# Performance work log

Hardware: AMD Instinct MI355X
Metric: run time of the kernel (lower is better)

The kernel has to match this reference:

```python
import jax, jax.numpy as jnp
import numpy as np

D_MODEL = 1024
N_HEADS = 16
HEAD_DIM = D_MODEL // N_HEADS  # 64


def _rotate_half(x):
    x1, x2 = jnp.split(x, 2, axis=-1)
    return jnp.concatenate((-x2, x1), axis=-1)


def setup_inputs() -> dict:
    key = jax.random.key(0)
    ks = jax.random.split(key, 9)
    B, S = 2, 2048
    sc = 1.0 / np.sqrt(D_MODEL)
    return {
        "x": jax.random.normal(ks[0], (B, S, D_MODEL), dtype=jnp.float32),
        "Wq": jax.random.normal(ks[1], (D_MODEL, D_MODEL), dtype=jnp.float32) * sc,
        "bq": jax.random.normal(ks[2], (D_MODEL,), dtype=jnp.float32) * 0.02,
        "Wk": jax.random.normal(ks[3], (D_MODEL, D_MODEL), dtype=jnp.float32) * sc,
        "bk": jax.random.normal(ks[4], (D_MODEL,), dtype=jnp.float32) * 0.02,
        "Wv": jax.random.normal(ks[5], (D_MODEL, D_MODEL), dtype=jnp.float32) * sc,
        "bv": jax.random.normal(ks[6], (D_MODEL,), dtype=jnp.float32) * 0.02,
        "Wo": jax.random.normal(ks[7], (D_MODEL, D_MODEL), dtype=jnp.float32) * sc,
        "bo": jax.random.normal(ks[8], (D_MODEL,), dtype=jnp.float32) * 0.02,
    }


def reference(x, Wq, bq, Wk, bk, Wv, bv, Wo, bo):
    B, S, _ = x.shape
    H, D = N_HEADS, HEAD_DIM
    # QKV projections -> [B, H, S, D]
    q = (x @ Wq + bq).reshape(B, S, H, D).transpose(0, 2, 1, 3)
    k = (x @ Wk + bk).reshape(B, S, H, D).transpose(0, 2, 1, 3)
    v = (x @ Wv + bv).reshape(B, S, H, D).transpose(0, 2, 1, 3)
    # Rotary embedding on head_dim
    inv_freq = 1.0 / (10000.0 ** (jnp.arange(0, D, 2, dtype=jnp.float32) / D))
    t = jnp.arange(S, dtype=jnp.float32)
    freqs = jnp.outer(t, inv_freq)                      # [S, D/2]
    emb = jnp.concatenate((freqs, freqs), axis=-1)      # [S, D]
    # Faithful to torch: cos/sin end up rank-5 [1,1,1,S,D], promoting q/k to [1,B,H,S,D]
    cos = jnp.cos(emb)[None, None, None]
    sin = jnp.sin(emb)[None, None, None]
    qe = q * cos + _rotate_half(q) * sin                # [1,B,H,S,D]
    ke = k * cos + _rotate_half(k) * sin                # [1,B,H,S,D]
    scores = jnp.matmul(qe, jnp.swapaxes(ke, -1, -2)) / np.sqrt(D).astype(np.float32)  # [1,B,H,S,S]
    attn = jax.nn.softmax(scores, axis=-1)
    out = jnp.matmul(attn, v)                           # [1,B,H,S,D] (v broadcast)
    # Faithful replication of torch transpose(1,2).contiguous().view(B,S,d_model)
    out = out.transpose(0, 2, 1, 3, 4).reshape(B, S, H * D)
    return out @ Wo + bo
```

## Files before the change

kernel.cpp:

```cpp
#include <hip/hip_runtime.h>
#include <hip/hip_bf16.h>
#include <stdint.h>

typedef __bf16 bf16;
typedef __bf16 bf16x8 __attribute__((ext_vector_type(8)));
typedef __bf16 bf16x4 __attribute__((ext_vector_type(4)));
typedef float  f32x4  __attribute__((ext_vector_type(4)));
typedef int    i32x4  __attribute__((ext_vector_type(4)));

#define MFMA16(a, b, c) __builtin_amdgcn_mfma_f32_16x16x32_bf16((a), (b), (c), 0, 0, 0)

#define GLOAD16(gp, lp) __builtin_amdgcn_global_load_lds(                     \
    (__attribute__((address_space(1))) void*)(gp),                            \
    (__attribute__((address_space(3))) void*)(lp), 16, 0, 0)


__global__ __launch_bounds__(256) void k_prep(
    const float* __restrict__ x,
    const float* __restrict__ Wq, const float* __restrict__ Wk,
    const float* __restrict__ Wv, const float* __restrict__ Wo,
    bf16* __restrict__ xb, bf16* __restrict__ wqkvt, bf16* __restrict__ wot,
    float* __restrict__ ct, float* __restrict__ st) {
    __shared__ float t[32][33];
    const int bid = blockIdx.x, tid = threadIdx.x;
    if (bid < 4096) {
        const int i = bid * 256 + tid;
        float4 v = ((const float4*)x)[i];
        bf16x4 o;
        o[0] = (bf16)v.x; o[1] = (bf16)v.y; o[2] = (bf16)v.z; o[3] = (bf16)v.w;
        ((bf16x4*)xb)[i] = o;
    } else if (bid < 4352) {
        const int i = (bid - 4096) * 256 + tid;
        const int s = i >> 5, j = i & 31;
        const float inv = expf(-(float)j * (9.210340371976184f / 32.0f));
        const float a = (float)s * inv;
        ct[i] = cosf(a);
        st[i] = sinf(a);
    } else {
        const int wb = bid - 4352;
        const int z = wb >> 10, tb = wb & 1023;
        const float* src = (z == 0) ? Wq : (z == 1) ? Wk : (z == 2) ? Wv : Wo;
        bf16* dst = (z < 3) ? wqkvt + (size_t)z * 1024 * 1024 : wot;
        const int bx = (tb & 31) * 32, by = (tb >> 5) * 32;
        const int tx = tid & 31, ty = tid >> 5;
#pragma unroll
        for (int i = 0; i < 32; i += 8)
            t[ty + i][tx] = src[(size_t)(by + ty + i) * 1024 + bx + tx];
        __syncthreads();
#pragma unroll
        for (int i = 0; i < 32; i += 8)
            dst[(size_t)(bx + ty + i) * 1024 + by + tx] = (bf16)t[tx][ty + i];
    }
}

__device__ __forceinline__ void gemm_loop(const bf16* __restrict__ A,
                                          const bf16* __restrict__ Bt,
                                          int m0, int n0,
                                          bf16* As, bf16* Bs,
                                          f32x4 (&acc)[4][4]) {
    const int tid  = threadIdx.x;
    const int w    = tid >> 6, lane = tid & 63;
    const int wr   = (w >> 1) * 64, wc = (w & 1) * 64;
    const int l15  = lane & 15, l4 = lane >> 4;
    const int srow = w * 16 + (lane >> 2);
    const int skol = 8 * ((lane & 3) ^ ((lane >> 3) & 3));
    const int rdb  = l15 * 32 + 8 * (l4 ^ ((l15 >> 1) & 3));
    const bf16* Ap = A  + (size_t)(m0 + srow) * 1024 + skol;
    const bf16* Bp = Bt + (size_t)(n0 + srow) * 1024 + skol;

#define GSTAGE(B, kt) do {                                                   \
        GLOAD16(Ap + (kt),         As + (B) * 4096 + w * 512);               \
        GLOAD16(Ap + 65536 + (kt), As + (B) * 4096 + 2048 + w * 512);        \
        GLOAD16(Bp + (kt),         Bs + (B) * 4096 + w * 512);               \
        GLOAD16(Bp + 65536 + (kt), Bs + (B) * 4096 + 2048 + w * 512);        \
    } while (0)

#define GTILE(t, B) do {                                                     \
        asm volatile("s_waitcnt vmcnt(0)" ::: "memory");                     \
        __builtin_amdgcn_s_barrier();                                        \
        if ((t) < 31) GSTAGE((B) ^ 1, ((t) + 1) * 32);                       \
        bf16x8 af[4], bfv[4];                                                \
        _Pragma("unroll")                                                    \
        for (int m = 0; m < 4; ++m)                                          \
            af[m] = *(const bf16x8*)(As + (B) * 4096 + (wr + 16 * m) * 32 + rdb); \
        _Pragma("unroll")                                                    \
        for (int n = 0; n < 4; ++n)                                          \
            bfv[n] = *(const bf16x8*)(Bs + (B) * 4096 + (wc + 16 * n) * 32 + rdb); \
        __builtin_amdgcn_s_setprio(1);                                       \
        _Pragma("unroll")                                                    \
        for (int m = 0; m < 4; ++m)                                          \
            _Pragma("unroll")                                                \
            for (int n = 0; n < 4; ++n)                                      \
                acc[m][n] = MFMA16(af[m], bfv[n], acc[m][n]);                \
        __builtin_amdgcn_s_setprio(0);                                       \
    } while (0)

    GSTAGE(0, 0);
    for (int t = 0; t < 32; t += 2) {
        GTILE(t, 0);
        GTILE(t + 1, 1);
    }
#undef GTILE
#undef GSTAGE
}

__global__ __launch_bounds__(256) void k_gemm_qkv(
    const bf16* __restrict__ X, const bf16* __restrict__ Wt,
    const float* __restrict__ bq, const float* __restrict__ bk,
    const float* __restrict__ bv,
    const float* __restrict__ ct, const float* __restrict__ st,
    bf16* __restrict__ qbuf, bf16* __restrict__ kbuf, bf16* __restrict__ vtb) {
    __shared__ __align__(16) bf16 As[2 * 4096];
    __shared__ __align__(16) bf16 Bs[2 * 4096];
    f32x4 acc[4][4] = {};
    const int nwg = gridDim.x * gridDim.y;
    const int wg  = blockIdx.y * gridDim.x + blockIdx.x;
    const int sw  = (wg & 7) * (nwg >> 3) + (wg >> 3);
    const int m0 = (sw / gridDim.x) * 128, n0 = (sw % gridDim.x) * 128;
    gemm_loop(X, Wt, m0, n0, As, Bs, acc);

    const int tid = threadIdx.x;
    const int w = tid >> 6, lane = tid & 63;
    const int wr = (w >> 1) * 64, wc = (w & 1) * 64;
    const int l15 = lane & 15, l4 = lane >> 4;

    const int featbase = n0 + wc;
    const int kind = featbase >> 10;
    const int col0 = featbase & 1023;
    const int h = col0 >> 6;
    const float* bias = (kind == 0) ? bq : (kind == 1) ? bk : bv;
    const float oscale = (kind == 0) ? 0.18033688011112042f : 1.0f;

#pragma unroll
    for (int m = 0; m < 4; ++m) {
#pragma unroll
        for (int j = 0; j < 4; ++j) {
            const int tok = m0 + wr + 16 * m + 4 * l4 + j;
            const int b = tok >> 11, s = tok & 2047;
            float vals[4];
#pragma unroll
            for (int n = 0; n < 4; ++n)
                vals[n] = acc[m][n][j] + bias[col0 + 16 * n + l15];
            if (kind < 2) {
                bf16* dst = (kind == 0) ? qbuf : kbuf;
                const size_t base = ((size_t)((b * 16 + h) * 2048 + s)) * 64;
#pragma unroll
                for (int n = 0; n < 4; ++n) {
                    const int dd = 16 * n + l15;
                    const int jr = dd & 31;
                    const float c = ct[s * 32 + jr], sn = st[s * 32 + jr];
                    const float other = vals[n ^ 2];
                    const float rot = (dd < 32) ? -other : other;
                    dst[base + dd] = (bf16)((vals[n] * c + rot * sn) * oscale);
                }
            } else {
                const int sp = (s & ~63) | ((s & 0x1C) << 1) | ((s & 0x20) >> 3) | (s & 3);
#pragma unroll
                for (int n = 0; n < 4; ++n) {
                    const int dd = 16 * n + l15;
                    vtb[((size_t)((b * 16 + h) * 64 + dd)) * 2048 + sp] = (bf16)vals[n];
                }
            }
        }
    }
}

__global__ __launch_bounds__(512) void k_attn(const bf16* __restrict__ qbuf,
                                              const bf16* __restrict__ kbuf,
                                              const bf16* __restrict__ vtb,
                                              bf16* __restrict__ ob) {
    __shared__ __align__(16) bf16 smem[2 * 2 * 2 * 4096];

    const int tid = threadIdx.x, w = tid >> 6, lane = tid & 63;
    const int team = w >> 2, wt = w & 3;
    const int l15 = lane & 15, l4 = lane >> 4;

    const int sid = blockIdx.x;
    const int bh  = (sid & 7) * 4 + ((sid >> 3) >> 4);
    const int qb0 = ((sid >> 3) & 15) * 128;
    const int b = bh >> 4, h = bh & 15;

    const bf16* qp = qbuf + ((size_t)bh * 2048 + qb0 + wt * 32 + l15) * 64 + 8 * l4;
    i32x4 qr00 = *(const i32x4*)qp;
    i32x4 qr01 = *(const i32x4*)(qp + 32);
    i32x4 qr10 = *(const i32x4*)(qp + 16 * 64);
    i32x4 qr11 = *(const i32x4*)(qp + 16 * 64 + 32);
    asm volatile("" :: "v"(qr00), "v"(qr01), "v"(qr10), "v"(qr11));
    asm volatile("s_waitcnt vmcnt(0)" ::: "memory");
    bf16x8 aq[2][2];
    aq[0][0] = __builtin_bit_cast(bf16x8, qr00);
    aq[0][1] = __builtin_bit_cast(bf16x8, qr01);
    aq[1][0] = __builtin_bit_cast(bf16x8, qr10);
    aq[1][1] = __builtin_bit_cast(bf16x8, qr11);

    bf16x8 ones;
#pragma unroll
    for (int i = 0; i < 8; ++i) ones[i] = (bf16)1.0f;

    f32x4 ao[2][4] = {};
    f32x4 lacc[2] = {};
    const f32x4 zf = {0.f, 0.f, 0.f, 0.f};

    const int r8   = lane >> 3;
    const int skol = 8 * ((lane & 7) ^ r8);
    const int rdb  = l15 * 64 + 32 * ((l15 >> 2) & 1) + 8 * (l4 ^ (l15 & 3));
    const bf16* kp = kbuf + (size_t)bh * 131072 + (size_t)team * 65536
                   + (size_t)(wt * 8 + r8) * 64 + skol;
    const bf16* vp = vtb  + (size_t)bh * 131072 + (size_t)(wt * 8 + r8) * 2048
                   + team * 1024 + skol;
    bf16* sK = smem + team * 16384;
    bf16* sV = smem + team * 16384 + 8192;
    const bf16* pK0 = sK + rdb;
    const bf16* pK1 = sK + (rdb ^ 32);
    const bf16* pV0 = sV + rdb;
    const bf16* pV1 = sV + (rdb ^ 32);

#define STAGE(B, t) do {                                                  \
        GLOAD16(kp + (size_t)(t) * 4096,        sK + (B) * 4096 + wt * 512);        \
        GLOAD16(kp + (size_t)(t) * 4096 + 2048, sK + (B) * 4096 + 2048 + wt * 512); \
        GLOAD16(vp + (t) * 64,                  sV + (B) * 4096 + wt * 512);        \
        GLOAD16(vp + 65536 + (t) * 64,          sV + (B) * 4096 + 2048 + wt * 512); \
    } while (0)

#define TILE(t, B) do {                                                       \
        asm volatile("s_waitcnt vmcnt(0)" ::: "memory");                      \
        __builtin_amdgcn_s_barrier();                                         \
        if ((t) < 15) STAGE((B) ^ 1, (t) + 1);                                \
        bf16x8 kfr[2][4], vfr[2][4];                                          \
        _Pragma("unroll")                                                     \
        for (int n = 0; n < 4; ++n) {                                         \
            kfr[0][n] = *(const bf16x8*)(pK0 + (B) * 4096 + n * 1024);        \
            kfr[1][n] = *(const bf16x8*)(pK1 + (B) * 4096 + n * 1024);        \
            vfr[0][n] = *(const bf16x8*)(pV0 + (B) * 4096 + n * 1024);        \
            vfr[1][n] = *(const bf16x8*)(pV1 + (B) * 4096 + n * 1024);        \
        }                                                                     \
        f32x4 sc[2][4];                                                       \
        __builtin_amdgcn_s_setprio(1);                                        \
        _Pragma("unroll")                                                     \
        for (int n = 0; n < 4; ++n) {                                         \
            sc[0][n] = MFMA16(kfr[0][n], aq[0][0], zf);                       \
            sc[1][n] = MFMA16(kfr[0][n], aq[1][0], zf);                       \
        }                                                                     \
        _Pragma("unroll")                                                     \
        for (int n = 0; n < 4; ++n) {                                         \
            sc[0][n] = MFMA16(kfr[1][n], aq[0][1], sc[0][n]);                 \
            sc[1][n] = MFMA16(kfr[1][n], aq[1][1], sc[1][n]);                 \
        }                                                                     \
        __builtin_amdgcn_s_setprio(0);                                        \
                  \
        bf16x8 ap[2][2];                                                      \
        _Pragma("unroll")                                                     \
        for (int f = 0; f < 2; ++f) {                                         \
            float e0[4], e1[4], e2[4], e3[4];                                 \
            _Pragma("unroll")                                                 \
            for (int r = 0; r < 4; ++r) {                                     \
                asm("v_exp_f32 %0, %1" : "=v"(e0[r]) : "v"(sc[f][0][r]));     \
                asm("v_exp_f32 %0, %1" : "=v"(e1[r]) : "v"(sc[f][1][r]));     \
                asm("v_exp_f32 %0, %1" : "=v"(e2[r]) : "v"(sc[f][2][r]));     \
                asm("v_exp_f32 %0, %1" : "=v"(e3[r]) : "v"(sc[f][3][r]));     \
            }                                                                 \
            unsigned q0, q1, q2, q3, q4, q5, q6, q7;                          \
            asm("v_cvt_pk_bf16_f32 %0, %1, %2" : "=v"(q0) : "v"(e0[0]), "v"(e0[1])); \
            asm("v_cvt_pk_bf16_f32 %0, %1, %2" : "=v"(q1) : "v"(e0[2]), "v"(e0[3])); \
            asm("v_cvt_pk_bf16_f32 %0, %1, %2" : "=v"(q2) : "v"(e2[0]), "v"(e2[1])); \
            asm("v_cvt_pk_bf16_f32 %0, %1, %2" : "=v"(q3) : "v"(e2[2]), "v"(e2[3])); \
            asm("v_cvt_pk_bf16_f32 %0, %1, %2" : "=v"(q4) : "v"(e1[0]), "v"(e1[1])); \
            asm("v_cvt_pk_bf16_f32 %0, %1, %2" : "=v"(q5) : "v"(e1[2]), "v"(e1[3])); \
            asm("v_cvt_pk_bf16_f32 %0, %1, %2" : "=v"(q6) : "v"(e3[0]), "v"(e3[1])); \
            asm("v_cvt_pk_bf16_f32 %0, %1, %2" : "=v"(q7) : "v"(e3[2]), "v"(e3[3])); \
            i32x4 w0 = {(int)q0, (int)q1, (int)q2, (int)q3};                  \
            i32x4 w1 = {(int)q4, (int)q5, (int)q6, (int)q7};                  \
            ap[f][0] = __builtin_bit_cast(bf16x8, w0);                        \
            ap[f][1] = __builtin_bit_cast(bf16x8, w1);                        \
        }                                                                     \
        __builtin_amdgcn_s_setprio(1);                                        \
        lacc[0] = MFMA16(ap[0][0], ones, lacc[0]);                            \
        lacc[0] = MFMA16(ap[0][1], ones, lacc[0]);                            \
        lacc[1] = MFMA16(ap[1][0], ones, lacc[1]);                            \
        lacc[1] = MFMA16(ap[1][1], ones, lacc[1]);                            \
        _Pragma("unroll")                                                     \
        for (int kk = 0; kk < 2; ++kk)                                        \
            _Pragma("unroll")                                                 \
            for (int n = 0; n < 4; ++n) {                                     \
                ao[0][n] = MFMA16(ap[0][kk], vfr[kk][n], ao[0][n]);           \
                ao[1][n] = MFMA16(ap[1][kk], vfr[kk][n], ao[1][n]);           \
            }                                                                 \
        __builtin_amdgcn_s_setprio(0);                                        \
    } while (0)

    STAGE(0, 0);
    for (int t = 0; t < 16; t += 2) {
        TILE(t, 0);
        TILE(t + 1, 1);
    }
#undef TILE
#undef STAGE

    float* mO = (float*)(smem + 16384);
    float* mL = (float*)smem;
    __syncthreads();
    if (team == 1) {
#pragma unroll
        for (int f = 0; f < 2; ++f) {
#pragma unroll
            for (int j = 0; j < 4; ++j) {
                const int row = wt * 32 + f * 16 + 4 * l4 + j;
#pragma unroll
                for (int n = 0; n < 4; ++n)
                    mO[row * 64 + 16 * n + l15] = ao[f][n][j];
                if (l15 == 0) mL[row] = lacc[f][j];
            }
        }
    }
    __syncthreads();
    if (team == 0) {
#pragma unroll
        for (int f = 0; f < 2; ++f) {
#pragma unroll
            for (int j = 0; j < 4; ++j) {
                const int row = wt * 32 + f * 16 + 4 * l4 + j;
                const float inv = 1.0f / (lacc[f][j] + mL[row]);
                const int s = qb0 + row;
                const size_t base = ((size_t)(h * 256 + b * 128 + (s >> 4))) * 1024
                                  + (s & 15) * 64;
#pragma unroll
                for (int n = 0; n < 4; ++n)
                    ob[base + 16 * n + l15] =
                        (bf16)((ao[f][n][j] + mO[row * 64 + 16 * n + l15]) * inv);
            }
        }
    }
}

__global__ __launch_bounds__(256) void k_gemm_out(const bf16* __restrict__ O,
                                                  const bf16* __restrict__ Wt,
                                                  const float* __restrict__ bo,
                                                  float* __restrict__ out) {
    __shared__ __align__(16) bf16 As[3 * 4096];
    __shared__ __align__(16) bf16 Bs[3 * 2048];
    f32x4 acc[4][2] = {};

    const int nwg = gridDim.x * gridDim.y;
    const int wg  = blockIdx.y * gridDim.x + blockIdx.x;
    const int sw  = (wg & 7) * (nwg >> 3) + (wg >> 3);
    const int m0 = (sw / gridDim.x) * 128, n0 = (sw % gridDim.x) * 64;

    const int tid  = threadIdx.x;
    const int w    = tid >> 6, lane = tid & 63;
    const int wr   = (w >> 1) * 64, wc = (w & 1) * 32;
    const int l15  = lane & 15, l4 = lane >> 4;
    const int srow = w * 16 + (lane >> 2);
    const int skol = 8 * ((lane & 3) ^ ((lane >> 3) & 3));
    const int rdb  = l15 * 32 + 8 * (l4 ^ ((l15 >> 1) & 3));
    const bf16* Ap = O  + (size_t)(m0 + srow) * 1024 + skol;
    const bf16* Bp = Wt + (size_t)(n0 + srow) * 1024 + skol;

#define OSTAGE(B, kt) do {                                                   \
        GLOAD16(Ap + (kt),         As + (B) * 4096 + w * 512);               \
        GLOAD16(Ap + 65536 + (kt), As + (B) * 4096 + 2048 + w * 512);        \
        GLOAD16(Bp + (kt),         Bs + (B) * 2048 + w * 512);               \
    } while (0)

#define OCOMP(B) do {                                                        \
        bf16x8 af[4], bfv[2];                                                \
        _Pragma("unroll")                                                    \
        for (int m = 0; m < 4; ++m)                                          \
            af[m] = *(const bf16x8*)(As + (B) * 4096 + (wr + 16 * m) * 32 + rdb); \
        _Pragma("unroll")                                                    \
        for (int n = 0; n < 2; ++n)                                          \
            bfv[n] = *(const bf16x8*)(Bs + (B) * 2048 + (wc + 16 * n) * 32 + rdb); \
        __builtin_amdgcn_s_setprio(1);                                       \
        _Pragma("unroll")                                                    \
        for (int m = 0; m < 4; ++m)                                          \
            _Pragma("unroll")                                                \
            for (int n = 0; n < 2; ++n)                                      \
                acc[m][n] = MFMA16(af[m], bfv[n], acc[m][n]);                \
        __builtin_amdgcn_s_setprio(0);                                       \
    } while (0)

    OSTAGE(0, 0);
    OSTAGE(1, 32);
    for (int i = 0; i < 30; i += 3) {
        asm volatile("s_waitcnt vmcnt(3)" ::: "memory");
        __builtin_amdgcn_s_barrier();
        OSTAGE(2, (i + 2) * 32);
        OCOMP(0);
        asm volatile("s_waitcnt vmcnt(3)" ::: "memory");
        __builtin_amdgcn_s_barrier();
        OSTAGE(0, (i + 3) * 32);
        OCOMP(1);
        asm volatile("s_waitcnt vmcnt(3)" ::: "memory");
        __builtin_amdgcn_s_barrier();
        OSTAGE(1, (i + 4) * 32);
        OCOMP(2);
    }
    asm volatile("s_waitcnt vmcnt(3)" ::: "memory");
    __builtin_amdgcn_s_barrier();
    OCOMP(0);
    asm volatile("s_waitcnt vmcnt(0)" ::: "memory");
    __builtin_amdgcn_s_barrier();
    OCOMP(1);
#undef OCOMP
#undef OSTAGE

#pragma unroll
    for (int m = 0; m < 4; ++m) {
#pragma unroll
        for (int j = 0; j < 4; ++j) {
            const int tok = m0 + wr + 16 * m + 4 * l4 + j;
#pragma unroll
            for (int n = 0; n < 2; ++n) {
                const int feat = n0 + wc + 16 * n + l15;
                out[(size_t)tok * 1024 + feat] = acc[m][n][j] + bo[feat];
            }
        }
    }
}

extern "C" void kernel_launch(void* const* d_in, const int* in_sizes, int n_in,
                              void* d_out, int out_size, void* d_ws, size_t ws_size,
                              hipStream_t stream) {
    (void)in_sizes; (void)n_in; (void)out_size; (void)ws_size;
    const float* x  = (const float*)d_in[0];
    const float* Wq = (const float*)d_in[1];
    const float* bq = (const float*)d_in[2];
    const float* Wk = (const float*)d_in[3];
    const float* bk = (const float*)d_in[4];
    const float* Wv = (const float*)d_in[5];
    const float* bv = (const float*)d_in[6];
    const float* Wo = (const float*)d_in[7];
    const float* bo = (const float*)d_in[8];
    float* out = (float*)d_out;

    char* p = (char*)d_ws;
    bf16* xb    = (bf16*)p;  p += (size_t)4096 * 1024 * 2;
    bf16* wqkvt = (bf16*)p;  p += (size_t)3072 * 1024 * 2;
    bf16* wot   = (bf16*)p;  p += (size_t)1024 * 1024 * 2;
    bf16* qbuf  = (bf16*)p;  p += (size_t)32 * 2048 * 64 * 2;
    bf16* kbuf  = (bf16*)p;  p += (size_t)32 * 2048 * 64 * 2;
    bf16* vtb   = (bf16*)p;  p += (size_t)32 * 64 * 2048 * 2;
    float* ct   = (float*)p; p += (size_t)2048 * 32 * 4;
    float* st   = (float*)p; p += (size_t)2048 * 32 * 4;
    bf16* obuf  = xb;

    k_prep<<<dim3(8448), dim3(256), 0, stream>>>(x, Wq, Wk, Wv, Wo,
                                                 xb, wqkvt, wot, ct, st);
    k_gemm_qkv<<<dim3(24, 32), dim3(256), 0, stream>>>(xb, wqkvt, bq, bk, bv,
                                                       ct, st, qbuf, kbuf, vtb);
    k_attn<<<dim3(512), dim3(512), 0, stream>>>(qbuf, kbuf, vtb, obuf);
    k_gemm_out<<<dim3(16, 32), dim3(256), 0, stream>>>(obuf, wot, bo, out);
}
```

Measured before the change: 118.4 us.

## Enlarge QKV GEMM tiles to 256x256 with 512 threads and staged pipelining

The QKV projection GEMM moves from 128x128 tiles with 4 waves to 256x256 tiles with 8 waves, and the K-step grows to 64. Each iteration is split into four MFMA phases, with the A-tile and B-tile prefetches issued between them, so loads overlap compute inside each tile. The LDS swizzle and launch grid are updated to match, and the block-index swizzle is made one-dimensional. The aim is more data reuse per LDS byte and less global traffic, but the grid shrinks to 192 blocks, which leaves some CUs idle and raises register and LDS pressure per block.

```diff
diff --git a/kernel.cpp b/kernel.cpp
--- a/kernel.cpp
+++ b/kernel.cpp
@@ -53,78 +53,131 @@
     }
 }
 
-__device__ __forceinline__ void gemm_loop(const bf16* __restrict__ A,
-                                          const bf16* __restrict__ Bt,
-                                          int m0, int n0,
-                                          bf16* As, bf16* Bs,
-                                          f32x4 (&acc)[4][4]) {
-    const int tid  = threadIdx.x;
-    const int w    = tid >> 6, lane = tid & 63;
-    const int wr   = (w >> 1) * 64, wc = (w & 1) * 64;
-    const int l15  = lane & 15, l4 = lane >> 4;
-    const int srow = w * 16 + (lane >> 2);
-    const int skol = 8 * ((lane & 3) ^ ((lane >> 3) & 3));
-    const int rdb  = l15 * 32 + 8 * (l4 ^ ((l15 >> 1) & 3));
-    const bf16* Ap = A  + (size_t)(m0 + srow) * 1024 + skol;
-    const bf16* Bp = Bt + (size_t)(n0 + srow) * 1024 + skol;
-
-#define GSTAGE(B, kt) do {                                                   \
-        GLOAD16(Ap + (kt),         As + (B) * 4096 + w * 512);               \
-        GLOAD16(Ap + 65536 + (kt), As + (B) * 4096 + 2048 + w * 512);        \
-        GLOAD16(Bp + (kt),         Bs + (B) * 4096 + w * 512);               \
-        GLOAD16(Bp + 65536 + (kt), Bs + (B) * 4096 + 2048 + w * 512);        \
-    } while (0)
-
-#define GTILE(t, B) do {                                                     \
-        asm volatile("s_waitcnt vmcnt(0)" ::: "memory");                     \
-        __builtin_amdgcn_s_barrier();                                        \
-        if ((t) < 31) GSTAGE((B) ^ 1, ((t) + 1) * 32);                       \
-        bf16x8 af[4], bfv[4];                                                \
-        _Pragma("unroll")                                                    \
-        for (int m = 0; m < 4; ++m)                                          \
-            af[m] = *(const bf16x8*)(As + (B) * 4096 + (wr + 16 * m) * 32 + rdb); \
-        _Pragma("unroll")                                                    \
-        for (int n = 0; n < 4; ++n)                                          \
-            bfv[n] = *(const bf16x8*)(Bs + (B) * 4096 + (wc + 16 * n) * 32 + rdb); \
-        __builtin_amdgcn_s_setprio(1);                                       \
-        _Pragma("unroll")                                                    \
-        for (int m = 0; m < 4; ++m)                                          \
-            _Pragma("unroll")                                                \
-            for (int n = 0; n < 4; ++n)                                      \
-                acc[m][n] = MFMA16(af[m], bfv[n], acc[m][n]);                \
-        __builtin_amdgcn_s_setprio(0);                                       \
-    } while (0)
-
-    GSTAGE(0, 0);
-    for (int t = 0; t < 32; t += 2) {
-        GTILE(t, 0);
-        GTILE(t + 1, 1);
-    }
-#undef GTILE
-#undef GSTAGE
-}
-
-__global__ __launch_bounds__(256) void k_gemm_qkv(
+__global__ __launch_bounds__(512) void k_gemm_qkv(
     const bf16* __restrict__ X, const bf16* __restrict__ Wt,
     const float* __restrict__ bq, const float* __restrict__ bk,
     const float* __restrict__ bv,
     const float* __restrict__ ct, const float* __restrict__ st,
     bf16* __restrict__ qbuf, bf16* __restrict__ kbuf, bf16* __restrict__ vtb) {
-    __shared__ __align__(16) bf16 As[2 * 4096];
-    __shared__ __align__(16) bf16 Bs[2 * 4096];
-    f32x4 acc[4][4] = {};
-    const int nwg = gridDim.x * gridDim.y;
-    const int wg  = blockIdx.y * gridDim.x + blockIdx.x;
-    const int sw  = (wg & 7) * (nwg >> 3) + (wg >> 3);
-    const int m0 = (sw / gridDim.x) * 128, n0 = (sw % gridDim.x) * 128;
-    gemm_loop(X, Wt, m0, n0, As, Bs, acc);
+    __shared__ __align__(16) bf16 As[2 * 16384];
+    __shared__ __align__(16) bf16 Bs[2 * 16384];
+    f32x4 acc[8][4] = {};
+
+    const int wg = blockIdx.x;
+    const int sw = (wg & 7) * 24 + (wg >> 3);
+    const int m0 = (sw / 12) * 256, n0 = (sw % 12) * 256;
 
     const int tid = threadIdx.x;
     const int w = tid >> 6, lane = tid & 63;
-    const int wr = (w >> 1) * 64, wc = (w & 1) * 64;
+    const int wm = w >> 2, wn = w & 3;
     const int l15 = lane & 15, l4 = lane >> 4;
-
-    const int featbase = n0 + wc;
+    const int skol = 8 * ((lane & 7) ^ (lane >> 3));
+    const int c0   = (8 * l4) ^ (8 * (l15 & 7));
+
+    const bf16* Ap = X  + (size_t)(m0 + (tid >> 3)) * 1024 + skol;
+    const bf16* Bp = Wt + (size_t)(n0 + (tid >> 3)) * 1024 + skol;
+    bf16* Ad = As + tid * 8;
+    bf16* Bd = Bs + tid * 8;
+    const bf16* pA0 = As + (wm * 128 + l15) * 64 + c0;
+    const bf16* pA1 = As + (wm * 128 + l15) * 64 + (c0 ^ 32);
+    const bf16* pB0 = Bs + (wn * 64 + l15) * 64 + c0;
+    const bf16* pB1 = Bs + (wn * 64 + l15) * 64 + (c0 ^ 32);
+
+#define ASTG(B, kt) do {                                                     \
+        GLOAD16(Ap + (kt),          Ad + (B) * 16384);                       \
+        GLOAD16(Ap + 65536 + (kt),  Ad + (B) * 16384 + 4096);                \
+        GLOAD16(Ap + 131072 + (kt), Ad + (B) * 16384 + 8192);                \
+        GLOAD16(Ap + 196608 + (kt), Ad + (B) * 16384 + 12288);               \
+    } while (0)
+#define BSTG(B, kt) do {                                                     \
+        GLOAD16(Bp + (kt),          Bd + (B) * 16384);                       \
+        GLOAD16(Bp + 65536 + (kt),  Bd + (B) * 16384 + 4096);                \
+        GLOAD16(Bp + 131072 + (kt), Bd + (B) * 16384 + 8192);                \
+        GLOAD16(Bp + 196608 + (kt), Bd + (B) * 16384 + 12288);               \
+    } while (0)
+
+#define QTILE(t, B) do {                                                      \
+        asm volatile("s_waitcnt vmcnt(0)" ::: "memory");                      \
+        __builtin_amdgcn_s_barrier();                                         \
+        bf16x8 af[8][2], bfv[4][2];                                           \
+             \
+        _Pragma("unroll")                                                     \
+        for (int m = 0; m < 4; ++m) {                                         \
+            af[m][0] = *(const bf16x8*)(pA0 + (B) * 16384 + m * 1024);        \
+            af[m][1] = *(const bf16x8*)(pA1 + (B) * 16384 + m * 1024);        \
+        }                                                                     \
+        _Pragma("unroll")                                                     \
+        for (int n = 0; n < 2; ++n) {                                         \
+            bfv[n][0] = *(const bf16x8*)(pB0 + (B) * 16384 + n * 1024);       \
+            bfv[n][1] = *(const bf16x8*)(pB1 + (B) * 16384 + n * 1024);       \
+        }                                                                     \
+        if ((t) < 15) ASTG((B) ^ 1, ((t) + 1) * 64);                          \
+        __builtin_amdgcn_s_setprio(1);                                        \
+        _Pragma("unroll")                                                     \
+        for (int m = 0; m < 4; ++m)                                           \
+            _Pragma("unroll")                                                 \
+            for (int n = 0; n < 2; ++n) {                                     \
+                acc[m][n] = MFMA16(af[m][0], bfv[n][0], acc[m][n]);           \
+                acc[m][n] = MFMA16(af[m][1], bfv[n][1], acc[m][n]);           \
+            }                                                                 \
+        __builtin_amdgcn_s_setprio(0);                                        \
+        __builtin_amdgcn_s_barrier();                                         \
+                       \
+        _Pragma("unroll")                                                     \
+        for (int n = 2; n < 4; ++n) {                                         \
+            bfv[n][0] = *(const bf16x8*)(pB0 + (B) * 16384 + n * 1024);       \
+            bfv[n][1] = *(const bf16x8*)(pB1 + (B) * 16384 + n * 1024);       \
+        }                                                                     \
+        if ((t) < 15) BSTG((B) ^ 1, ((t) + 1) * 64);                          \
+        __builtin_amdgcn_s_setprio(1);                                        \
+        _Pragma("unroll")                                                     \
+        for (int m = 0; m < 4; ++m)                                           \
+            _Pragma("unroll")                                                 \
+            for (int n = 2; n < 4; ++n) {                                     \
+                acc[m][n] = MFMA16(af[m][0], bfv[n][0], acc[m][n]);           \
+                acc[m][n] = MFMA16(af[m][1], bfv[n][1], acc[m][n]);           \
+            }                                                                 \
+        __builtin_amdgcn_s_setprio(0);                                        \
+        __builtin_amdgcn_s_barrier();                                         \
+                                      \
+        _Pragma("unroll")                                                     \
+        for (int m = 4; m < 8; ++m) {                                         \
+            af[m][0] = *(const bf16x8*)(pA0 + (B) * 16384 + m * 1024);        \
+            af[m][1] = *(const bf16x8*)(pA1 + (B) * 16384 + m * 1024);        \
+        }                                                                     \
+        __builtin_amdgcn_s_setprio(1);                                        \
+        _Pragma("unroll")                                                     \
+        for (int m = 4; m < 8; ++m)                                           \
+            _Pragma("unroll")                                                 \
+            for (int n = 2; n < 4; ++n) {                                     \
+                acc[m][n] = MFMA16(af[m][0], bfv[n][0], acc[m][n]);           \
+                acc[m][n] = MFMA16(af[m][1], bfv[n][1], acc[m][n]);           \
+            }                                                                 \
+        __builtin_amdgcn_s_setprio(0);                                        \
+        __builtin_amdgcn_s_barrier();                                         \
+                     \
+        __builtin_amdgcn_s_setprio(1);                                        \
+        _Pragma("unroll")                                                     \
+        for (int m = 4; m < 8; ++m)                                           \
+            _Pragma("unroll")                                                 \
+            for (int n = 0; n < 2; ++n) {                                     \
+                acc[m][n] = MFMA16(af[m][0], bfv[n][0], acc[m][n]);           \
+                acc[m][n] = MFMA16(af[m][1], bfv[n][1], acc[m][n]);           \
+            }                                                                 \
+        __builtin_amdgcn_s_setprio(0);                                        \
+    } while (0)
+
+    ASTG(0, 0);
+    BSTG(0, 0);
+    for (int t = 0; t < 16; t += 2) {
+        QTILE(t, 0);
+        QTILE(t + 1, 1);
+    }
+#undef QTILE
+#undef BSTG
+#undef ASTG
+
+    const int featbase = n0 + wn * 64;
     const int kind = featbase >> 10;
     const int col0 = featbase & 1023;
     const int h = col0 >> 6;
@@ -132,10 +185,10 @@
     const float oscale = (kind == 0) ? 0.18033688011112042f : 1.0f;
 
 #pragma unroll
-    for (int m = 0; m < 4; ++m) {
+    for (int m = 0; m < 8; ++m) {
 #pragma unroll
         for (int j = 0; j < 4; ++j) {
-            const int tok = m0 + wr + 16 * m + 4 * l4 + j;
+            const int tok = m0 + wm * 128 + 16 * m + 4 * l4 + j;
             const int b = tok >> 11, s = tok & 2047;
             float vals[4];
 #pragma unroll
@@ -445,8 +498,8 @@
 
     k_prep<<<dim3(8448), dim3(256), 0, stream>>>(x, Wq, Wk, Wv, Wo,
                                                  xb, wqkvt, wot, ct, st);
-    k_gemm_qkv<<<dim3(24, 32), dim3(256), 0, stream>>>(xb, wqkvt, bq, bk, bv,
-                                                       ct, st, qbuf, kbuf, vtb);
+    k_gemm_qkv<<<dim3(192), dim3(512), 0, stream>>>(xb, wqkvt, bq, bk, bv,
+                                                    ct, st, qbuf, kbuf, vtb);
     k_attn<<<dim3(512), dim3(512), 0, stream>>>(qbuf, kbuf, vtb, obuf);
     k_gemm_out<<<dim3(16, 32), dim3(256), 0, stream>>>(obuf, wot, bo, out);
 }
```

New measurement: 129.4 us (median of 2 runs). 9.2% more time.
